# Performance work log

Measured on AMD Instinct MI355X. Metric: run time of the kernel, lower is better.

Reference implementation:

```python
import jax, jax.numpy as jnp
import numpy as np

D_MODEL = 1024
NUM_HEADS = 16
THETA = 10000.0


def _trunc_normal(key, shape):
    # matches torch.nn.init.trunc_normal_(std=std, a=-3*std, b=3*std)
    std = (2.0 / (shape[0] + shape[1])) ** 0.5
    return jax.random.truncated_normal(key, -3.0, 3.0, shape, dtype=jnp.float32) * std


def setup_inputs() -> dict:
    key = jax.random.key(0)
    kx, kq, kk, kv, ko = jax.random.split(key, 5)
    B, S, D = 2, 2048, D_MODEL
    return {
        "x": jax.random.normal(kx, (B, S, D), dtype=jnp.float32),
        "Wq": _trunc_normal(kq, (D, D)),  # torch Linear weight: [out, in]
        "Wk": _trunc_normal(kk, (D, D)),
        "Wv": _trunc_normal(kv, (D, D)),
        "Wo": _trunc_normal(ko, (D, D)),
        "token_positions": jnp.arange(S, dtype=jnp.int32),
    }


def _rope(x, token_positions):
    # x: [B, H, S, d_k]; RoPE on interleaved pairs (k r) with r=2
    d_k = x.shape[-1]
    inv_freq = THETA ** (-2.0 * jnp.arange(d_k // 2, dtype=jnp.float32) / d_k)
    ang = token_positions.astype(jnp.float32)[:, None] * inv_freq[None, :]  # [S, d_k/2]
    sin, cos = jnp.sin(ang).astype(x.dtype), jnp.cos(ang).astype(x.dtype)
    x0, x1 = x[..., 0::2], x[..., 1::2]
    y0 = x0 * cos - x1 * sin
    y1 = x0 * sin + x1 * cos
    return jnp.stack([y0, y1], axis=-1).reshape(x.shape)


def reference(x, Wq, Wk, Wv, Wo, token_positions):
    B, S, D = x.shape
    H = NUM_HEADS
    d_k = D // H

    def proj(W):  # y = x @ W^T, split heads -> [B, H, S, d_k]
        y = jnp.einsum('bsd,ed->bse', x, W)
        return y.reshape(B, S, H, d_k).transpose(0, 2, 1, 3)

    q = _rope(proj(Wq), token_positions)
    k = _rope(proj(Wk), token_positions)
    v = proj(Wv)

    # causal mask: attend where pos_k <= pos_q
    mask = token_positions[None, :] <= token_positions[:, None]  # [S_q, S_k]
    logits = jnp.einsum('bhqd,bhkd->bhqk', q, k) / (d_k ** 0.5)
    logits = jnp.where(mask, logits, -jnp.inf)
    scores = jax.nn.softmax(logits, axis=-1)
    attn = jnp.einsum('bhqk,bhkd->bhqd', scores, v)  # [B, H, S, d_k]
    attn = attn.transpose(0, 2, 1, 3).reshape(B, S, D)
    return jnp.einsum('bsd,ed->bse', attn, Wo)
```

## Files before the change

kernel.cpp:

```cpp
#include <hip/hip_runtime.h>
#include <hip/hip_bf16.h>

typedef __attribute__((ext_vector_type(8))) short s16x8;
typedef __attribute__((ext_vector_type(4))) float f32x4;

__device__ __forceinline__ unsigned short f2b(float x) {
  unsigned int u = __float_as_uint(x);
  u = (u + 0x7fffu + ((u >> 16) & 1u)) >> 16;
  return (unsigned short)u;
}

__device__ __forceinline__ unsigned int pkbf(float a, float b) {
  return (unsigned int)f2b(a) | ((unsigned int)f2b(b) << 16);
}

__device__ __forceinline__ float b2f(unsigned short u) {
  return __uint_as_float((unsigned int)u << 16);
}

__device__ __forceinline__ void gl2lds16(const unsigned short* g, unsigned short* lds) {
  __builtin_amdgcn_global_load_lds(
      (const __attribute__((address_space(1))) unsigned int*)g,
      (__attribute__((address_space(3))) unsigned int*)lds, 16, 0, 0);
}

__global__ __launch_bounds__(256) void cast_all(
    const float* __restrict__ x,  const float* __restrict__ Wq,
    const float* __restrict__ Wk, const float* __restrict__ Wv,
    const float* __restrict__ Wo, unsigned short* __restrict__ dst) {
  int i = blockIdx.x * 256 + threadIdx.x;
  const float* src;
  int off;
  if (i < 1048576) { src = x; off = i; }
  else {
    int j = i - 1048576;
    int seg = j >> 18;
    off = j & 262143;
    src = (seg == 0) ? Wq : (seg == 1) ? Wk : (seg == 2) ? Wv : Wo;
  }
  const float4 v = ((const float4*)src)[off];
  ushort4 o;
  o.x = f2b(v.x); o.y = f2b(v.y); o.z = f2b(v.z); o.w = f2b(v.w);
  ((ushort4*)dst)[i] = o;
}

#define BM 128
#define BN 128
#define KDIM 1024

__global__ __launch_bounds__(256) void gemm_qkv(
    const unsigned short* __restrict__ A,
    const unsigned short* __restrict__ Bt,
    const int* __restrict__ tok,
    unsigned short* __restrict__ Qo,
    unsigned short* __restrict__ Ko,
    unsigned short* __restrict__ Vt) {
  __shared__ unsigned short As[BM * 64];
  __shared__ unsigned short Bs[BN * 64];
  const int tid = threadIdx.x;
  const int bid = blockIdx.x;
  const int xcd = bid & 7;
  const int loc = bid >> 3;
  const int m0 = (loc / 3) * BM;
  const int n0 = (xcd * 3 + loc % 3) * BN;
  const int w = tid >> 6, lane = tid & 63;
  const int ln = lane & 15, quad = lane >> 4;
  const int wm = (w >> 1) * 64, wn = (w & 1) * 64;

  const int srow = w * 32 + (lane >> 3);
  const int sg = (lane & 7) ^ (lane >> 3);
  const int rs = ln & 7;

  const f32x4 zero = {0.f, 0.f, 0.f, 0.f};
  f32x4 acc[4][4];
#pragma unroll
  for (int i = 0; i < 4; ++i)
#pragma unroll
    for (int j = 0; j < 4; ++j) acc[i][j] = zero;

  for (int kb = 0; kb < KDIM / 64; ++kb) {
    __syncthreads();
#pragma unroll
    for (int t = 0; t < 4; ++t) {
      gl2lds16(A  + (size_t)(m0 + srow + t * 8) * KDIM + kb * 64 + sg * 8, &As[(w * 32 + t * 8) * 64]);
      gl2lds16(Bt + (size_t)(n0 + srow + t * 8) * KDIM + kb * 64 + sg * 8, &Bs[(w * 32 + t * 8) * 64]);
    }
    __syncthreads();
#pragma unroll
    for (int ks = 0; ks < 2; ++ks) {
      s16x8 af[4], bfr[4];
#pragma unroll
      for (int i = 0; i < 4; ++i)
        af[i] = *(const s16x8*)(&As[(wm + i * 16 + ln) * 64 + (((ks * 4 + quad) ^ rs) * 8)]);
#pragma unroll
      for (int j = 0; j < 4; ++j)
        bfr[j] = *(const s16x8*)(&Bs[(wn + j * 16 + ln) * 64 + (((ks * 4 + quad) ^ rs) * 8)]);
#pragma unroll
      for (int i = 0; i < 4; ++i)
#pragma unroll
        for (int j = 0; j < 4; ++j)
          acc[i][j] = __builtin_amdgcn_mfma_f32_16x16x32_bf16(af[i], bfr[j], acc[i][j], 0, 0, 0);
    }
  }

#pragma unroll
  for (int j = 0; j < 4; ++j) {
    int gn = n0 + wn + j * 16 + ln;
    bool isV = (gn >= 2048);
    int e = isV ? (gn - 2048) : (gn & 1023);
    int h = e >> 6, d = e & 63;
    float inv = __expf(-0.2878231366f * (float)(d >> 1));
#pragma unroll
    for (int i = 0; i < 4; ++i) {
      int gmb = m0 + wm + i * 16 + quad * 4;
#pragma unroll
      for (int r = 0; r < 4; ++r) {
        float val = acc[i][j][r];
        float part = __shfl_xor(val, 1, 64);
        int m = gmb + r;
        int b = m >> 11, s = m & 2047;
        if (!isV) {
          float pos = (float)tok[s];
          float ang = pos * inv;
          float sn, cs;
          __sincosf(ang, &sn, &cs);
          float x0 = (d & 1) ? part : val;
          float x1 = (d & 1) ? val : part;
          float y = (d & 1) ? (x0 * sn + x1 * cs) : (x0 * cs - x1 * sn);
          unsigned short* dst = (gn < 1024) ? Qo : Ko;
          dst[(((size_t)b * 16 + h) * 2048 + s) * 64 + d] = f2b(y);
        } else {
          Vt[(((size_t)b * 16 + h) * 64 + d) * 2048 + s] = f2b(val);
        }
      }
    }
  }
}

__global__ __launch_bounds__(256, 3) void attn_partial(
    const unsigned short* __restrict__ Q,
    const unsigned short* __restrict__ K,
    const unsigned short* __restrict__ Vt,
    unsigned short* __restrict__ Opart,
    float2* __restrict__ ML) {
  __shared__ unsigned short Ks[64 * 64];
  __shared__ unsigned short Vs[64 * 64];
  __shared__ unsigned short Pt[4][16 * 72];

  const int bid = blockIdx.x;
  const int xcd = bid & 7;
  const int loc = bid >> 3;
  const int bh = xcd * 4 + (loc & 3);
  const int widx = loc >> 2;
  int c, qh;
  if (widx < 28) {
    if (widx < 13)      { c = 0; qh = 3 + widx; }
    else if (widx < 22) { c = 1; qh = 7 + (widx - 13); }
    else if (widx < 27) { c = 2; qh = 11 + (widx - 22); }
    else                { c = 3; qh = 15; }
  } else {
    int s = widx - 28;
    int wt = s >> 2;
    c = s & 3;
    qh = 4 * c + 2 - wt;
  }
  const int kbeg = c * 512;
  const int khi = min(kbeg + 512, qh * 128 + 128);

  const int tid = threadIdx.x;
  const int w = tid >> 6, lane = tid & 63;
  const int ln = lane & 15, quad = lane >> 4;
  const int qb = qh * 128 + w * 32;

  const unsigned short* Qb = Q + (size_t)bh * 2048 * 64;
  const unsigned short* Kb = K + (size_t)bh * 2048 * 64;
  const unsigned short* Vb = Vt + (size_t)bh * 64 * 2048;

  const int srow = w * 16 + (lane >> 3);
  const int sg = (lane & 7) ^ (srow & 7);

  s16x8 bq[2][2];
#pragma unroll
  for (int u = 0; u < 2; ++u)
#pragma unroll
    for (int hh = 0; hh < 2; ++hh)
      bq[u][hh] = *(const s16x8*)(&Qb[(size_t)(qb + u * 16 + ln) * 64 + hh * 32 + quad * 8]);

  const f32x4 zero = {0.f, 0.f, 0.f, 0.f};
  f32x4 o[2][4];
#pragma unroll
  for (int u = 0; u < 2; ++u)
#pragma unroll
    for (int j = 0; j < 4; ++j) o[u][j] = zero;
  float m_i[2] = {-3e38f, -3e38f};
  float l_i[2] = {0.f, 0.f};

  const int rdsw = ((ln & 7) * 8);

  for (int k0 = kbeg; k0 < khi; k0 += 64) {
    __syncthreads();
    gl2lds16(Kb + (size_t)(k0 + srow) * 64 + sg * 8,       &Ks[(w * 16) * 64]);
    gl2lds16(Kb + (size_t)(k0 + srow + 8) * 64 + sg * 8,   &Ks[(w * 16 + 8) * 64]);
    gl2lds16(Vb + (size_t)srow * 2048 + k0 + sg * 8,       &Vs[(w * 16) * 64]);
    gl2lds16(Vb + (size_t)(srow + 8) * 2048 + k0 + sg * 8, &Vs[(w * 16 + 8) * 64]);
    __syncthreads();

    s16x8 ka[4][2];
#pragma unroll
    for (int t = 0; t < 4; ++t)
#pragma unroll
      for (int hh = 0; hh < 2; ++hh)
        ka[t][hh] = *(const s16x8*)(&Ks[(t * 16 + ln) * 64 + (((hh * 4 + quad) * 8) ^ rdsw)]);

#pragma unroll
    for (int u = 0; u < 2; ++u) {
      const int q = qb + u * 16 + ln;
      f32x4 st[4];
#pragma unroll
      for (int t = 0; t < 4; ++t) {
        f32x4 s = __builtin_amdgcn_mfma_f32_16x16x32_bf16(ka[t][0], bq[u][0], zero, 0, 0, 0);
        st[t] = __builtin_amdgcn_mfma_f32_16x16x32_bf16(ka[t][1], bq[u][1], s, 0, 0, 0);
      }
      float lm = -3e38f;
#pragma unroll
      for (int t = 0; t < 4; ++t)
#pragma unroll
        for (int r = 0; r < 4; ++r) {
          int kk = k0 + t * 16 + quad * 4 + r;
          float v = st[t][r] * 0.125f;
          v = (kk > q) ? -3e38f : v;
          st[t][r] = v;
          lm = fmaxf(lm, v);
        }
      lm = fmaxf(lm, __shfl_xor(lm, 16, 64));
      lm = fmaxf(lm, __shfl_xor(lm, 32, 64));
      float mn = fmaxf(m_i[u], lm);
      float al = __expf(m_i[u] - mn);
      float rs = 0.f;
#pragma unroll
      for (int t = 0; t < 4; ++t)
#pragma unroll
        for (int r = 0; r < 4; ++r) {
          float p = __expf(st[t][r] - mn);
          st[t][r] = p;
          rs += p;
        }
      rs += __shfl_xor(rs, 16, 64);
      rs += __shfl_xor(rs, 32, 64);
      m_i[u] = mn;
      l_i[u] = l_i[u] * al + rs;
#pragma unroll
      for (int j = 0; j < 4; ++j) o[u][j] *= al;

#pragma unroll
      for (int t = 0; t < 4; ++t) {
        uint2 pv;
        pv.x = pkbf(st[t][0], st[t][1]);
        pv.y = pkbf(st[t][2], st[t][3]);
        *(uint2*)(&Pt[w][ln * 72 + t * 16 + quad * 4]) = pv;
      }
      __builtin_amdgcn_wave_barrier();
#pragma unroll
      for (int hh = 0; hh < 2; ++hh) {
        s16x8 pb = *(const s16x8*)(&Pt[w][ln * 72 + hh * 32 + quad * 8]);
#pragma unroll
        for (int j = 0; j < 4; ++j) {
          s16x8 va = *(const s16x8*)(&Vs[(j * 16 + ln) * 64 + (((hh * 4 + quad) * 8) ^ rdsw)]);
          o[u][j] = __builtin_amdgcn_mfma_f32_16x16x32_bf16(va, pb, o[u][j], 0, 0, 0);
        }
      }
      __builtin_amdgcn_wave_barrier();
    }
  }

#pragma unroll
  for (int u = 0; u < 2; ++u) {
    int s = qb + u * 16 + ln;
    size_t row = ((size_t)bh * 4 + c) * 2048 + s;
    if (quad == 0) ML[row] = make_float2(m_i[u], l_i[u]);
    size_t base = row * 64;
#pragma unroll
    for (int j = 0; j < 4; ++j) {
      ushort4 o4;
      o4.x = f2b(o[u][j][0]);
      o4.y = f2b(o[u][j][1]);
      o4.z = f2b(o[u][j][2]);
      o4.w = f2b(o[u][j][3]);
      *(ushort4*)(&Opart[base + j * 16 + quad * 4]) = o4;
    }
  }
}

__global__ __launch_bounds__(256) void attn_merge(
    const unsigned short* __restrict__ Opart,
    const float2* __restrict__ ML,
    unsigned short* __restrict__ Ao) {
  int idx = blockIdx.x * 256 + threadIdx.x;
  int d0 = (idx & 7) * 8;
  int q  = (idx >> 3) & 2047;
  int bh = idx >> 14;
  int nc = (q >> 9) + 1;

  float m_c[4], l_c[4];
  float M = -3e38f;
  for (int c = 0; c < nc; ++c) {
    float2 ml = ML[((size_t)bh * 4 + c) * 2048 + q];
    m_c[c] = ml.x; l_c[c] = ml.y;
    M = fmaxf(M, ml.x);
  }
  float acc[8] = {0, 0, 0, 0, 0, 0, 0, 0};
  float L = 0.f;
  for (int c = 0; c < nc; ++c) {
    float wc = __expf(m_c[c] - M);
    L += wc * l_c[c];
    const ushort4* p = (const ushort4*)(Opart + (((size_t)bh * 4 + c) * 2048 + q) * 64 + d0);
    ushort4 a = p[0], bvec = p[1];
    acc[0] += wc * b2f(a.x); acc[1] += wc * b2f(a.y);
    acc[2] += wc * b2f(a.z); acc[3] += wc * b2f(a.w);
    acc[4] += wc * b2f(bvec.x); acc[5] += wc * b2f(bvec.y);
    acc[6] += wc * b2f(bvec.z); acc[7] += wc * b2f(bvec.w);
  }
  float invL = 1.0f / L;
  int b = bh >> 4, h = bh & 15;
  unsigned short* dst = Ao + ((size_t)b * 2048 + q) * 1024 + h * 64 + d0;
  ushort4 o0, o1;
  o0.x = f2b(acc[0] * invL); o0.y = f2b(acc[1] * invL);
  o0.z = f2b(acc[2] * invL); o0.w = f2b(acc[3] * invL);
  o1.x = f2b(acc[4] * invL); o1.y = f2b(acc[5] * invL);
  o1.z = f2b(acc[6] * invL); o1.w = f2b(acc[7] * invL);
  ((ushort4*)dst)[0] = o0;
  ((ushort4*)dst)[1] = o1;
}

__global__ __launch_bounds__(256) void gemm_out(
    const unsigned short* __restrict__ A,
    const unsigned short* __restrict__ Bt,
    float* __restrict__ out) {
  __shared__ unsigned short As[BM * 64];
  __shared__ unsigned short Bs[BN * 64];
  const int tid = threadIdx.x;
  const int bid = blockIdx.x;
  const int m0 = (bid >> 3) * BM;
  const int n0 = (bid & 7) * BN;
  const int w = tid >> 6, lane = tid & 63;
  const int ln = lane & 15, quad = lane >> 4;
  const int wm = (w >> 1) * 64, wn = (w & 1) * 64;

  const int srow = w * 32 + (lane >> 3);
  const int sg = (lane & 7) ^ (lane >> 3);
  const int rs = ln & 7;

  const f32x4 zero = {0.f, 0.f, 0.f, 0.f};
  f32x4 acc[4][4];
#pragma unroll
  for (int i = 0; i < 4; ++i)
#pragma unroll
    for (int j = 0; j < 4; ++j) acc[i][j] = zero;

  for (int kb = 0; kb < KDIM / 64; ++kb) {
    __syncthreads();
#pragma unroll
    for (int t = 0; t < 4; ++t) {
      gl2lds16(A  + (size_t)(m0 + srow + t * 8) * KDIM + kb * 64 + sg * 8, &As[(w * 32 + t * 8) * 64]);
      gl2lds16(Bt + (size_t)(n0 + srow + t * 8) * KDIM + kb * 64 + sg * 8, &Bs[(w * 32 + t * 8) * 64]);
    }
    __syncthreads();
#pragma unroll
    for (int ks = 0; ks < 2; ++ks) {
      s16x8 af[4], bfr[4];
#pragma unroll
      for (int i = 0; i < 4; ++i)
        af[i] = *(const s16x8*)(&As[(wm + i * 16 + ln) * 64 + (((ks * 4 + quad) ^ rs) * 8)]);
#pragma unroll
      for (int j = 0; j < 4; ++j)
        bfr[j] = *(const s16x8*)(&Bs[(wn + j * 16 + ln) * 64 + (((ks * 4 + quad) ^ rs) * 8)]);
#pragma unroll
      for (int i = 0; i < 4; ++i)
#pragma unroll
        for (int j = 0; j < 4; ++j)
          acc[i][j] = __builtin_amdgcn_mfma_f32_16x16x32_bf16(af[i], bfr[j], acc[i][j], 0, 0, 0);
    }
  }
#pragma unroll
  for (int i = 0; i < 4; ++i) {
    int gmb = m0 + wm + i * 16 + quad * 4;
#pragma unroll
    for (int j = 0; j < 4; ++j) {
      int gn = n0 + wn + j * 16 + ln;
#pragma unroll
      for (int r = 0; r < 4; ++r)
        out[(size_t)(gmb + r) * 1024 + gn] = acc[i][j][r];
    }
  }
}

extern "C" void kernel_launch(void* const* d_in, const int* in_sizes, int n_in,
                              void* d_out, int out_size, void* d_ws, size_t ws_size,
                              hipStream_t stream) {
  const float* x  = (const float*)d_in[0];
  const float* Wq = (const float*)d_in[1];
  const float* Wk = (const float*)d_in[2];
  const float* Wv = (const float*)d_in[3];
  const float* Wo = (const float*)d_in[4];
  const int* tok  = (const int*)d_in[5];
  float* out = (float*)d_out;

  char* ws = (char*)d_ws;
  unsigned short* xb    = (unsigned short*)(ws);
  unsigned short* Wcat  = (unsigned short*)(ws + (8ull  << 20));
  unsigned short* Wob   = (unsigned short*)(ws + (14ull << 20));
  unsigned short* Qb    = (unsigned short*)(ws + (16ull << 20));
  unsigned short* Kb    = (unsigned short*)(ws + (24ull << 20));
  unsigned short* Vtb   = (unsigned short*)(ws + (32ull << 20));
  unsigned short* Ab    = (unsigned short*)(ws + (40ull << 20));
  unsigned short* Opart = (unsigned short*)(ws + (48ull << 20));
  float2*         ML    = (float2*)        (ws + (80ull << 20));

  cast_all<<<dim3(8192), dim3(256), 0, stream>>>(x, Wq, Wk, Wv, Wo, xb);
  gemm_qkv<<<dim3(768), dim3(256), 0, stream>>>(xb, Wcat, tok, Qb, Kb, Vtb);
  attn_partial<<<dim3(1280), dim3(256), 0, stream>>>(Qb, Kb, Vtb, Opart, ML);
  attn_merge<<<dim3(2048), dim3(256), 0, stream>>>(Opart, ML, Ab);
  gemm_out<<<dim3(256), dim3(256), 0, stream>>>(Ab, Wob, out);
}
```

Before: 221.3 us.

## Double-buffer LDS tiles with K-step 32 in QKV and output GEMMs

```diff
diff --git a/kernel.cpp b/kernel.cpp
--- a/kernel.cpp
+++ b/kernel.cpp
@@ -44,32 +44,30 @@
   ((ushort4*)dst)[i] = o;
 }
 
-#define BM 128
-#define BN 128
 #define KDIM 1024
 
-__global__ __launch_bounds__(256) void gemm_qkv(
+__global__ __launch_bounds__(256, 4) void gemm_qkv(
     const unsigned short* __restrict__ A,
     const unsigned short* __restrict__ Bt,
     const int* __restrict__ tok,
     unsigned short* __restrict__ Qo,
     unsigned short* __restrict__ Ko,
     unsigned short* __restrict__ Vt) {
-  __shared__ unsigned short As[BM * 64];
-  __shared__ unsigned short Bs[BN * 64];
+  __shared__ unsigned short As[2][128 * 32];
+  __shared__ unsigned short Bs[2][128 * 32];
   const int tid = threadIdx.x;
   const int bid = blockIdx.x;
   const int xcd = bid & 7;
   const int loc = bid >> 3;
-  const int m0 = (loc / 3) * BM;
-  const int n0 = (xcd * 3 + loc % 3) * BN;
+  const int m0 = (loc / 3) * 128;
+  const int n0 = (xcd * 3 + loc % 3) * 128;
   const int w = tid >> 6, lane = tid & 63;
   const int ln = lane & 15, quad = lane >> 4;
   const int wm = (w >> 1) * 64, wn = (w & 1) * 64;
 
-  const int srow = w * 32 + (lane >> 3);
-  const int sg = (lane & 7) ^ (lane >> 3);
-  const int rs = ln & 7;
+  const int rr = lane >> 2;
+  const int gsw = ((lane & 3) ^ ((rr ^ (rr >> 2)) & 3)) * 8;
+  const int sr = (ln ^ (ln >> 2)) & 3;
 
   const f32x4 zero = {0.f, 0.f, 0.f, 0.f};
   f32x4 acc[4][4];
@@ -78,30 +76,34 @@
 #pragma unroll
     for (int j = 0; j < 4; ++j) acc[i][j] = zero;
 
-  for (int kb = 0; kb < KDIM / 64; ++kb) {
+#define QKV_STAGE(kb, p)                                                              \
+  do {                                                                                \
+    int col = (kb) * 32 + gsw;                                                        \
+    gl2lds16(A  + (size_t)(m0 + w * 32 + rr) * KDIM + col,      &As[p][(w * 32) * 32]);      \
+    gl2lds16(A  + (size_t)(m0 + w * 32 + 16 + rr) * KDIM + col, &As[p][(w * 32 + 16) * 32]); \
+    gl2lds16(Bt + (size_t)(n0 + w * 32 + rr) * KDIM + col,      &Bs[p][(w * 32) * 32]);      \
+    gl2lds16(Bt + (size_t)(n0 + w * 32 + 16 + rr) * KDIM + col, &Bs[p][(w * 32 + 16) * 32]); \
+  } while (0)
+
+  QKV_STAGE(0, 0);
+  for (int kb = 0; kb < 32; ++kb) {
+    const int p = kb & 1;
     __syncthreads();
-#pragma unroll
-    for (int t = 0; t < 4; ++t) {
-      gl2lds16(A  + (size_t)(m0 + srow + t * 8) * KDIM + kb * 64 + sg * 8, &As[(w * 32 + t * 8) * 64]);
-      gl2lds16(Bt + (size_t)(n0 + srow + t * 8) * KDIM + kb * 64 + sg * 8, &Bs[(w * 32 + t * 8) * 64]);
-    }
-    __syncthreads();
-#pragma unroll
-    for (int ks = 0; ks < 2; ++ks) {
-      s16x8 af[4], bfr[4];
-#pragma unroll
-      for (int i = 0; i < 4; ++i)
-        af[i] = *(const s16x8*)(&As[(wm + i * 16 + ln) * 64 + (((ks * 4 + quad) ^ rs) * 8)]);
+    if (kb < 31) QKV_STAGE(kb + 1, p ^ 1);
+    s16x8 af[4], bfr[4];
+#pragma unroll
+    for (int i = 0; i < 4; ++i)
+      af[i] = *(const s16x8*)(&As[p][(wm + i * 16 + ln) * 32 + ((quad ^ sr) * 8)]);
+#pragma unroll
+    for (int j = 0; j < 4; ++j)
+      bfr[j] = *(const s16x8*)(&Bs[p][(wn + j * 16 + ln) * 32 + ((quad ^ sr) * 8)]);
+#pragma unroll
+    for (int i = 0; i < 4; ++i)
 #pragma unroll
       for (int j = 0; j < 4; ++j)
-        bfr[j] = *(const s16x8*)(&Bs[(wn + j * 16 + ln) * 64 + (((ks * 4 + quad) ^ rs) * 8)]);
-#pragma unroll
-      for (int i = 0; i < 4; ++i)
-#pragma unroll
-        for (int j = 0; j < 4; ++j)
-          acc[i][j] = __builtin_amdgcn_mfma_f32_16x16x32_bf16(af[i], bfr[j], acc[i][j], 0, 0, 0);
-    }
-  }
+        acc[i][j] = __builtin_amdgcn_mfma_f32_16x16x32_bf16(af[i], bfr[j], acc[i][j], 0, 0, 0);
+  }
+#undef QKV_STAGE
 
 #pragma unroll
   for (int j = 0; j < 4; ++j) {
@@ -332,23 +334,23 @@
   ((ushort4*)dst)[1] = o1;
 }
 
-__global__ __launch_bounds__(256) void gemm_out(
+__global__ __launch_bounds__(256, 3) void gemm_out(
     const unsigned short* __restrict__ A,
     const unsigned short* __restrict__ Bt,
     float* __restrict__ out) {
-  __shared__ unsigned short As[BM * 64];
-  __shared__ unsigned short Bs[BN * 64];
+  __shared__ unsigned short As[2][128 * 32];
+  __shared__ unsigned short Bs[2][128 * 32];
   const int tid = threadIdx.x;
   const int bid = blockIdx.x;
-  const int m0 = (bid >> 3) * BM;
-  const int n0 = (bid & 7) * BN;
+  const int m0 = (bid >> 3) * 128;
+  const int n0 = (bid & 7) * 128;
   const int w = tid >> 6, lane = tid & 63;
   const int ln = lane & 15, quad = lane >> 4;
   const int wm = (w >> 1) * 64, wn = (w & 1) * 64;
 
-  const int srow = w * 32 + (lane >> 3);
-  const int sg = (lane & 7) ^ (lane >> 3);
-  const int rs = ln & 7;
+  const int rr = lane >> 2;
+  const int gsw = ((lane & 3) ^ ((rr ^ (rr >> 2)) & 3)) * 8;
+  const int sr = (ln ^ (ln >> 2)) & 3;
 
   const f32x4 zero = {0.f, 0.f, 0.f, 0.f};
   f32x4 acc[4][4];
@@ -357,30 +359,35 @@
 #pragma unroll
     for (int j = 0; j < 4; ++j) acc[i][j] = zero;
 
-  for (int kb = 0; kb < KDIM / 64; ++kb) {
+#define OUT_STAGE(kb, p)                                                              \
+  do {                                                                                \
+    int col = (kb) * 32 + gsw;                                                        \
+    gl2lds16(A  + (size_t)(m0 + w * 32 + rr) * KDIM + col,      &As[p][(w * 32) * 32]);      \
+    gl2lds16(A  + (size_t)(m0 + w * 32 + 16 + rr) * KDIM + col, &As[p][(w * 32 + 16) * 32]); \
+    gl2lds16(Bt + (size_t)(n0 + w * 32 + rr) * KDIM + col,      &Bs[p][(w * 32) * 32]);      \
+    gl2lds16(Bt + (size_t)(n0 + w * 32 + 16 + rr) * KDIM + col, &Bs[p][(w * 32 + 16) * 32]); \
+  } while (0)
+
+  OUT_STAGE(0, 0);
+  for (int kb = 0; kb < 32; ++kb) {
+    const int p = kb & 1;
     __syncthreads();
-#pragma unroll
-    for (int t = 0; t < 4; ++t) {
-      gl2lds16(A  + (size_t)(m0 + srow + t * 8) * KDIM + kb * 64 + sg * 8, &As[(w * 32 + t * 8) * 64]);
-      gl2lds16(Bt + (size_t)(n0 + srow + t * 8) * KDIM + kb * 64 + sg * 8, &Bs[(w * 32 + t * 8) * 64]);
-    }
-    __syncthreads();
-#pragma unroll
-    for (int ks = 0; ks < 2; ++ks) {
-      s16x8 af[4], bfr[4];
-#pragma unroll
-      for (int i = 0; i < 4; ++i)
-        af[i] = *(const s16x8*)(&As[(wm + i * 16 + ln) * 64 + (((ks * 4 + quad) ^ rs) * 8)]);
+    if (kb < 31) OUT_STAGE(kb + 1, p ^ 1);
+    s16x8 af[4], bfr[4];
+#pragma unroll
+    for (int i = 0; i < 4; ++i)
+      af[i] = *(const s16x8*)(&As[p][(wm + i * 16 + ln) * 32 + ((quad ^ sr) * 8)]);
+#pragma unroll
+    for (int j = 0; j < 4; ++j)
+      bfr[j] = *(const s16x8*)(&Bs[p][(wn + j * 16 + ln) * 32 + ((quad ^ sr) * 8)]);
+#pragma unroll
+    for (int i = 0; i < 4; ++i)
 #pragma unroll
       for (int j = 0; j < 4; ++j)
-        bfr[j] = *(const s16x8*)(&Bs[(wn + j * 16 + ln) * 64 + (((ks * 4 + quad) ^ rs) * 8)]);
-#pragma unroll
-      for (int i = 0; i < 4; ++i)
-#pragma unroll
-        for (int j = 0; j < 4; ++j)
-          acc[i][j] = __builtin_amdgcn_mfma_f32_16x16x32_bf16(af[i], bfr[j], acc[i][j], 0, 0, 0);
-    }
-  }
+        acc[i][j] = __builtin_amdgcn_mfma_f32_16x16x32_bf16(af[i], bfr[j], acc[i][j], 0, 0, 0);
+  }
+#undef OUT_STAGE
+
 #pragma unroll
   for (int i = 0; i < 4; ++i) {
     int gmb = m0 + wm + i * 16 + quad * 4;
```

Result: faster. 212.3 us (-4.1%).
